# Optimization experiments

Hardware: AMD Instinct MI355X
Metric: run time of the kernel (lower is better)

Reference implementation:

```python
import jax, jax.numpy as jnp
import numpy as np

N_NODES = 50000
N_EDGES = 800000
N_RELS = 200
D = 128


def setup_inputs() -> dict:
    key = jax.random.key(0)
    ks = jax.random.split(key, 9)
    h = jax.random.normal(ks[0], (N_NODES, D), dtype=jnp.float32)
    r = jax.random.normal(ks[1], (N_RELS, D), dtype=jnp.float32)
    norm = jax.random.uniform(ks[2], (N_NODES, 1), dtype=jnp.float32)
    src = jax.random.randint(ks[3], (N_EDGES,), 0, N_NODES, dtype=jnp.int32)
    dst = jax.random.randint(ks[4], (N_EDGES,), 0, N_NODES, dtype=jnp.int32)
    rel = jax.random.randint(ks[5], (N_EDGES,), 0, N_RELS, dtype=jnp.int32)
    stdv = 1.0 / np.sqrt(D)
    W_msg = jax.random.uniform(ks[6], (D, D), minval=-stdv, maxval=stdv, dtype=jnp.float32)
    W = jax.random.uniform(ks[7], (D, D), minval=-stdv, maxval=stdv, dtype=jnp.float32)
    b = jax.random.uniform(ks[8], (D,), minval=-stdv, maxval=stdv, dtype=jnp.float32)
    return {"h": h, "r": r, "norm": norm, "src": src, "dst": dst, "rel": rel,
            "W_msg": W_msg, "W": W, "b": b}


def reference(h, r, norm, src, dst, rel, W_msg, W, b):
    # dropout=0.0 (eval); h = h * norm (symmetric-norm pre-scale)
    hn = h * norm                                    # [N, D]
    # per-edge message: (h_src - r_rel) @ W_msg
    msg = (hn[src] - r[rel]) @ W_msg                 # [E, D]
    # scatter-sum to destination nodes, then post-scale by norm
    agg = jax.ops.segment_sum(msg, dst, num_segments=hn.shape[0]) * norm  # [N, D]
    out = hn @ W + agg + b
    return jax.nn.relu(out)
```

## Files before the change

### kernel.cpp

```cpp
#include <hip/hip_runtime.h>

#define N_NODES 50000
#define N_EDGES 800000
#define DIM 128
#define K2 256
#define NREL 200
#define NB2 391
#define SLAB 3072
#define EPB 2048
#define FILL_BLOCKS ((N_EDGES + EPB - 1) / EPB)
#define BNF 16
#define NFB 3125
#define ECAP6 768

typedef unsigned short u16;
typedef __attribute__((ext_vector_type(8))) short short8;
typedef __attribute__((ext_vector_type(4))) float f32x4;

__device__ __forceinline__ float bf2f(u16 v) {
    union { unsigned int u; float f; } x;
    x.u = ((unsigned int)v) << 16;
    return x.f;
}

__device__ __forceinline__ u16 f2bf(float f) {
    union { unsigned int u; float f; } x;
    x.f = f;
    return (u16)((x.u + 0x7FFFu + ((x.u >> 16) & 1u)) >> 16);
}

__device__ __forceinline__ int sniff_fp32(const void* h, int tid) {
    const u16* hp = (const u16*)h;
    u16 v = hp[2 * (tid & 63)];
    float a = fabsf(bf2f(v));
    int insane = ((v & 0x7F80) == 0x7F80) || (a != 0.0f && (a > 1e6f || a < 1e-20f));
    return __popcll(__ballot(insane)) > 16;
}

#define PREP_H (N_NODES * 32)
#define PREP_R (NREL * 32)
#define PREP_W 8192
#define PREP_N (N_NODES / 4)
#define PREP_B 32
#define PREP_TOT (PREP_H + PREP_R + PREP_W + PREP_N + PREP_B)
#define PREP_BLK512 ((PREP_TOT + 511) / 512)
__global__ __launch_bounds__(512) void prep_fill(
    const void* __restrict__ h, const void* __restrict__ r, const void* __restrict__ norm,
    const void* __restrict__ W, const void* __restrict__ Wmsg, const void* __restrict__ bias,
    const int* __restrict__ dst, const int* __restrict__ src, const int* __restrict__ rel,
    u16* __restrict__ hx, u16* __restrict__ r_bf, u16* __restrict__ wt,
    u16* __restrict__ norm_bf, float* __restrict__ b_f,
    int* __restrict__ cursor, int* __restrict__ spk1)
{
    __shared__ int hist[NB2];
    __shared__ int lbase[NB2];
    __shared__ int gbase[NB2];
    __shared__ int sd[512];
    __shared__ int pay[EPB];
    __shared__ u16 bkt[EPB];
    int tid = threadIdx.x;

    if (blockIdx.x < FILL_BLOCKS) {
        for (int i = tid; i < NB2; i += 512) hist[i] = 0;
        __syncthreads();
        int e0 = blockIdx.x * EPB;
        int myb[4], myr[4], myp[4];
#pragma unroll
        for (int i = 0; i < 4; ++i) {
            int e = e0 + i * 512 + tid;
            myb[i] = -1;
            if (e < N_EDGES) {
                int d = dst[e];
                int b = d >> 7;
                myb[i] = b;
                myr[i] = atomicAdd(&hist[b], 1);
                myp[i] = src[e] | (rel[e] << 16) | ((d & 127) << 24);
            }
        }
        __syncthreads();
        sd[tid] = (tid < NB2) ? hist[tid] : 0;
        __syncthreads();
        for (int off = 1; off < 512; off <<= 1) {
            int v = (tid >= off) ? sd[tid - off] : 0;
            __syncthreads();
            sd[tid] += v;
            __syncthreads();
        }
        if (tid < NB2) {
            lbase[tid] = sd[tid] - hist[tid];
            gbase[tid] = tid * SLAB + (hist[tid] ? atomicAdd(&cursor[tid], hist[tid]) : 0);
        }
        __syncthreads();
#pragma unroll
        for (int i = 0; i < 4; ++i) {
            if (myb[i] >= 0) {
                int lp = lbase[myb[i]] + myr[i];
                pay[lp] = myp[i];
                bkt[lp] = (u16)myb[i];
            }
        }
        __syncthreads();
        int total = N_EDGES - e0; if (total > EPB) total = EPB;
#pragma unroll
        for (int i = 0; i < 4; ++i) {
            int lp = i * 512 + tid;
            if (lp < total) {
                int b = bkt[lp];
                spk1[gbase[b] + (lp - lbase[b])] = pay[lp];
            }
        }
        return;
    }

    int isf = sniff_fp32(h, tid);
    int t = (blockIdx.x - FILL_BLOCKS) * 512 + tid;
    if (t < PREP_H) {
        int n = t >> 5, c = t & 31;
        float4 v; float nv;
        if (isf) {
            nv = ((const float*)norm)[n];
            v = *(const float4*)((const float*)h + (size_t)n * DIM + c * 4);
        } else {
            nv = bf2f(((const u16*)norm)[n]);
            ushort4 u = *(const ushort4*)((const u16*)h + (size_t)n * DIM + c * 4);
            v = make_float4(bf2f(u.x), bf2f(u.y), bf2f(u.z), bf2f(u.w));
        }
        ushort4 o;
        o.x = f2bf(v.x * nv); o.y = f2bf(v.y * nv); o.z = f2bf(v.z * nv); o.w = f2bf(v.w * nv);
        *(ushort4*)(hx + (size_t)n * DIM + c * 4) = o;
    } else if (t < PREP_H + PREP_R) {
        int t2 = t - PREP_H;
        int rho = t2 >> 5, c = t2 & 31;
        float4 v;
        if (isf) v = *(const float4*)((const float*)r + (size_t)rho * DIM + c * 4);
        else {
            ushort4 u = *(const ushort4*)((const u16*)r + (size_t)rho * DIM + c * 4);
            v = make_float4(bf2f(u.x), bf2f(u.y), bf2f(u.z), bf2f(u.w));
        }
        ushort4 o;
        o.x = f2bf(v.x); o.y = f2bf(v.y); o.z = f2bf(v.z); o.w = f2bf(v.w);
        *(ushort4*)(r_bf + (size_t)rho * DIM + c * 4) = o;
    } else if (t < PREP_H + PREP_R + PREP_W) {
        int t3 = t - PREP_H - PREP_R;
        int j = t3 >> 6;
        int k0 = (t3 & 63) * 4;
        ushort4 o;
        u16* op = (u16*)&o;
        for (int kk = 0; kk < 4; ++kk) {
            int k = k0 + kk;
            float wv;
            if (isf) wv = (k < 128) ? ((const float*)W)[(size_t)k * DIM + j]
                                    : ((const float*)Wmsg)[(size_t)(k - 128) * DIM + j];
            else     wv = (k < 128) ? bf2f(((const u16*)W)[(size_t)k * DIM + j])
                                    : bf2f(((const u16*)Wmsg)[(size_t)(k - 128) * DIM + j]);
            op[kk] = f2bf(wv);
        }
        *(ushort4*)(wt + (size_t)j * K2 + k0) = o;
    } else if (t < PREP_H + PREP_R + PREP_W + PREP_N) {
        int n0 = (t - PREP_H - PREP_R - PREP_W) * 4;
        ushort4 o;
        if (isf) {
            float4 v = *(const float4*)((const float*)norm + n0);
            o.x = f2bf(v.x); o.y = f2bf(v.y); o.z = f2bf(v.z); o.w = f2bf(v.w);
        } else {
            o = *(const ushort4*)((const u16*)norm + n0);
        }
        *(ushort4*)(norm_bf + n0) = o;
    } else if (t < PREP_TOT) {
        int j0 = (t - PREP_H - PREP_R - PREP_W - PREP_N) * 4;
        float4 v;
        if (isf) v = *(const float4*)((const float*)bias + j0);
        else {
            ushort4 u = *(const ushort4*)((const u16*)bias + j0);
            v = make_float4(bf2f(u.x), bf2f(u.y), bf2f(u.z), bf2f(u.w));
        }
        *(float4*)(b_f + j0) = v;
    }
}

__global__ __launch_bounds__(512) void sort_fine(
    const int* __restrict__ cursor, const int* __restrict__ spk1,
    int* __restrict__ spk2, int* __restrict__ nodeBase)
{
    __shared__ int hist[128];
    __shared__ int lb[128];
    __shared__ int sd[512];
    __shared__ int sorted[SLAB];
    int tid = threadIdx.x;
    int fb = blockIdx.x;
    int acc = 0;
    for (int i = tid; i < NB2; i += 512)
        if (i < fb) acc += cursor[i];
    sd[tid] = acc;
    __syncthreads();
    for (int off = 256; off > 0; off >>= 1) {
        if (tid < off) sd[tid] += sd[tid + off];
        __syncthreads();
    }
    int base = sd[0];
    int size = cursor[fb];
    if (size > SLAB) size = SLAB;
    if (tid < 128) hist[tid] = 0;
    __syncthreads();
    int myp[6], myr[6], myd[6];
#pragma unroll
    for (int q = 0; q < 6; ++q) {
        int i = tid + q * 512;
        myd[q] = -1;
        if (i < size) {
            int pk = spk1[fb * SLAB + i];
            int dl = (pk >> 24) & 127;
            myp[q] = pk;
            myd[q] = dl;
            myr[q] = atomicAdd(&hist[dl], 1);
        }
    }
    __syncthreads();
    if (tid < 128) sd[tid] = hist[tid];
    __syncthreads();
    for (int off = 1; off < 128; off <<= 1) {
        int v = 0;
        if (tid < 128 && tid >= off) v = sd[tid - off];
        __syncthreads();
        if (tid < 128) sd[tid] += v;
        __syncthreads();
    }
    if (tid < 128) lb[tid] = sd[tid] - hist[tid];
    __syncthreads();
#pragma unroll
    for (int q = 0; q < 6; ++q)
        if (myd[q] >= 0) sorted[lb[myd[q]] + myr[q]] = myp[q];
    __syncthreads();
    for (int i = tid; i < size; i += 512) spk2[base + i] = sorted[i];
    if (tid < 128) {
        int node = fb * 128 + tid;
        if (node <= N_NODES) nodeBase[node] = base + lb[tid];
    }
    if (fb == 0 && tid == 0) nodeBase[N_NODES] = N_EDGES;
}

__global__ __launch_bounds__(256) void bucket_fused(
    const u16* __restrict__ hx, const u16* __restrict__ r_bf,
    const u16* __restrict__ norm_bf, const float* __restrict__ b_f,
    const int* __restrict__ nodeBase, const int* __restrict__ spk,
    const u16* __restrict__ wt, const void* __restrict__ h, void* __restrict__ out)
{
    __shared__ int nb[BNF + 1];
    __shared__ int eidx[ECAP6];
    __shared__ u16 Xu[BNF][136];
    int tid = threadIdx.x;
    int b = blockIdx.x;
    if (tid <= BNF) nb[tid] = nodeBase[b * BNF + tid];
    __syncthreads();
    int bs = nb[0];
    int tot = nb[BNF] - bs; if (tot > ECAP6) tot = ECAP6;
    for (int i = tid; i < tot; i += 256) eidx[i] = spk[bs + i];
    __syncthreads();

    int g = tid & 15, grp = tid >> 4;
    {
        int rs = nb[grp] - bs, re = nb[grp + 1] - bs;
        if (rs > ECAP6) rs = ECAP6;
        if (re > ECAP6) re = ECAP6;
        int cnt = re - rs;
        float acc[8] = {};
        int j = 0;
        for (; j + 3 < cnt; j += 4) {
            int pk0 = eidx[rs + j], pk1 = eidx[rs + j + 1];
            int pk2 = eidx[rs + j + 2], pk3 = eidx[rs + j + 3];
            short8 h0 = *(const short8*)(hx + (size_t)(pk0 & 0xFFFF) * DIM + g * 8);
            short8 h1 = *(const short8*)(hx + (size_t)(pk1 & 0xFFFF) * DIM + g * 8);
            short8 h2 = *(const short8*)(hx + (size_t)(pk2 & 0xFFFF) * DIM + g * 8);
            short8 h3 = *(const short8*)(hx + (size_t)(pk3 & 0xFFFF) * DIM + g * 8);
            short8 v0 = *(const short8*)(r_bf + (size_t)((pk0 >> 16) & 0xFF) * DIM + g * 8);
            short8 v1 = *(const short8*)(r_bf + (size_t)((pk1 >> 16) & 0xFF) * DIM + g * 8);
            short8 v2 = *(const short8*)(r_bf + (size_t)((pk2 >> 16) & 0xFF) * DIM + g * 8);
            short8 v3 = *(const short8*)(r_bf + (size_t)((pk3 >> 16) & 0xFF) * DIM + g * 8);
#pragma unroll
            for (int d = 0; d < 8; ++d) {
                acc[d] += (bf2f((u16)h0[d]) - bf2f((u16)v0[d]))
                        + (bf2f((u16)h1[d]) - bf2f((u16)v1[d]))
                        + (bf2f((u16)h2[d]) - bf2f((u16)v2[d]))
                        + (bf2f((u16)h3[d]) - bf2f((u16)v3[d]));
            }
        }
        for (; j < cnt; ++j) {
            int pk = eidx[rs + j];
            short8 hv = *(const short8*)(hx + (size_t)(pk & 0xFFFF) * DIM + g * 8);
            short8 rv = *(const short8*)(r_bf + (size_t)((pk >> 16) & 0xFF) * DIM + g * 8);
#pragma unroll
            for (int d = 0; d < 8; ++d) acc[d] += bf2f((u16)hv[d]) - bf2f((u16)rv[d]);
        }
        int node = b * BNF + grp;
        float nv = bf2f(norm_bf[node]);
        short8 o;
#pragma unroll
        for (int d = 0; d < 8; ++d) o[d] = (short)f2bf(acc[d] * nv);
        *(short8*)&Xu[grp][g * 8] = o;
    }
    __syncthreads();

    int w = tid >> 6, lane = tid & 63;
    int m = lane & 15, quad = lane >> 4;
    int nodeA = b * BNF + m;
    short8 a[8];
#pragma unroll
    for (int kb = 0; kb < 4; ++kb)
        a[kb] = *(const short8*)(hx + (size_t)nodeA * DIM + kb * 32 + quad * 8);
#pragma unroll
    for (int kb = 0; kb < 4; ++kb)
        a[4 + kb] = *(const short8*)&Xu[m][kb * 32 + quad * 8];
    int isf = sniff_fp32(h, tid);
#pragma unroll
    for (int ct = 0; ct < 2; ++ct) {
        int n0 = w * 32 + ct * 16;
        f32x4 c4 = {0.f, 0.f, 0.f, 0.f};
#pragma unroll
        for (int kb = 0; kb < 8; ++kb) {
            short8 bv = *(const short8*)(wt + (size_t)(n0 + m) * K2 + kb * 32 + quad * 8);
            c4 = __builtin_amdgcn_mfma_f32_16x16x32_bf16(a[kb], bv, c4, 0, 0, 0);
        }
        int col = n0 + m;
        float bb = b_f[col];
#pragma unroll
        for (int rg = 0; rg < 4; ++rg) {
            int n = b * BNF + quad * 4 + rg;
            float v = c4[rg] + bb;
            v = v > 0.f ? v : 0.f;
            if (isf) ((float*)out)[(size_t)n * DIM + col] = v;
            else     ((u16*)out)[(size_t)n * DIM + col] = f2bf(v);
        }
    }
}

static inline size_t alup(size_t x) { return (x + 255) & ~(size_t)255; }

extern "C" void kernel_launch(void* const* d_in, const int* in_sizes, int n_in,
                              void* d_out, int out_size, void* d_ws, size_t ws_size,
                              hipStream_t stream) {
    const void* h    = d_in[0];
    const void* r    = d_in[1];
    const void* norm = d_in[2];
    const int* src   = (const int*)d_in[3];
    const int* dst   = (const int*)d_in[4];
    const int* rel   = (const int*)d_in[5];
    const void* Wmsg = d_in[6];
    const void* W    = d_in[7];
    const void* b    = d_in[8];

    char* p = (char*)d_ws;
    u16* hx       = (u16*)p;                 p += alup((size_t)N_NODES * DIM * 2);
    u16* r_bf     = (u16*)p;                 p += alup((size_t)NREL * DIM * 2);
    u16* wt       = (u16*)p;                 p += alup((size_t)DIM * K2 * 2);
    u16* norm_bf  = (u16*)p;                 p += alup((size_t)N_NODES * 2);
    float* b_f    = (float*)p;               p += alup((size_t)DIM * 4);
    int* cursor   = (int*)p;                 p += alup((size_t)NB2 * 4);
    int* nodeBase = (int*)p;                 p += alup((size_t)(N_NODES + 64) * 4);
    int* spk1     = (int*)p;                 p += alup((size_t)NB2 * SLAB * 4);
    int* spk2     = (int*)p;                 p += alup((size_t)N_EDGES * 4);

    hipMemsetAsync(cursor, 0, (size_t)NB2 * 4, stream);
    prep_fill<<<FILL_BLOCKS + PREP_BLK512, 512, 0, stream>>>(
        h, r, norm, W, Wmsg, b, dst, src, rel,
        hx, r_bf, wt, norm_bf, b_f, cursor, spk1);
    sort_fine<<<NB2, 512, 0, stream>>>(cursor, spk1, spk2, nodeBase);
    bucket_fused<<<NFB, 256, 0, stream>>>(
        hx, r_bf, norm_bf, b_f, nodeBase, spk2, wt, h, d_out);
}
```

Measured before the change: 173.3 us.

## Fuse fine sort into aggregation kernel via per-block shared-memory bucketing

Removes the separate sort_fine kernel and the spk2/nodeBase buffers. Each aggregation block of 16 nodes now scans its coarse 128-node slab and uses shared-memory atomics to bucket the edges for its own 16 nodes, capping each node at DEGCAP=64 edges. This saves one kernel launch and a global write and read of the sorted edge list. In exchange every slab is read 8 times, once per sub-block, and nodes with more than 64 in-edges would be truncated. The order of edges within a node also becomes nondeterministic.

```diff
diff --git a/kernel.cpp b/kernel.cpp
--- a/kernel.cpp
+++ b/kernel.cpp
@@ -9,9 +9,8 @@
 #define SLAB 3072
 #define EPB 2048
 #define FILL_BLOCKS ((N_EDGES + EPB - 1) / EPB)
-#define BNF 16
-#define NFB 3125
-#define ECAP6 768
+#define NFB8 (NB2 * 8)
+#define DEGCAP 64
 
 typedef unsigned short u16;
 typedef __attribute__((ext_vector_type(8))) short short8;
@@ -178,96 +177,43 @@
     }
 }
 
-__global__ __launch_bounds__(512) void sort_fine(
-    const int* __restrict__ cursor, const int* __restrict__ spk1,
-    int* __restrict__ spk2, int* __restrict__ nodeBase)
-{
-    __shared__ int hist[128];
-    __shared__ int lb[128];
-    __shared__ int sd[512];
-    __shared__ int sorted[SLAB];
-    int tid = threadIdx.x;
-    int fb = blockIdx.x;
-    int acc = 0;
-    for (int i = tid; i < NB2; i += 512)
-        if (i < fb) acc += cursor[i];
-    sd[tid] = acc;
-    __syncthreads();
-    for (int off = 256; off > 0; off >>= 1) {
-        if (tid < off) sd[tid] += sd[tid + off];
-        __syncthreads();
-    }
-    int base = sd[0];
-    int size = cursor[fb];
-    if (size > SLAB) size = SLAB;
-    if (tid < 128) hist[tid] = 0;
-    __syncthreads();
-    int myp[6], myr[6], myd[6];
-#pragma unroll
-    for (int q = 0; q < 6; ++q) {
-        int i = tid + q * 512;
-        myd[q] = -1;
-        if (i < size) {
-            int pk = spk1[fb * SLAB + i];
-            int dl = (pk >> 24) & 127;
-            myp[q] = pk;
-            myd[q] = dl;
-            myr[q] = atomicAdd(&hist[dl], 1);
-        }
-    }
-    __syncthreads();
-    if (tid < 128) sd[tid] = hist[tid];
-    __syncthreads();
-    for (int off = 1; off < 128; off <<= 1) {
-        int v = 0;
-        if (tid < 128 && tid >= off) v = sd[tid - off];
-        __syncthreads();
-        if (tid < 128) sd[tid] += v;
-        __syncthreads();
-    }
-    if (tid < 128) lb[tid] = sd[tid] - hist[tid];
-    __syncthreads();
-#pragma unroll
-    for (int q = 0; q < 6; ++q)
-        if (myd[q] >= 0) sorted[lb[myd[q]] + myr[q]] = myp[q];
-    __syncthreads();
-    for (int i = tid; i < size; i += 512) spk2[base + i] = sorted[i];
-    if (tid < 128) {
-        int node = fb * 128 + tid;
-        if (node <= N_NODES) nodeBase[node] = base + lb[tid];
-    }
-    if (fb == 0 && tid == 0) nodeBase[N_NODES] = N_EDGES;
-}
-
 __global__ __launch_bounds__(256) void bucket_fused(
     const u16* __restrict__ hx, const u16* __restrict__ r_bf,
     const u16* __restrict__ norm_bf, const float* __restrict__ b_f,
-    const int* __restrict__ nodeBase, const int* __restrict__ spk,
+    const int* __restrict__ cursor, const int* __restrict__ spk1,
     const u16* __restrict__ wt, const void* __restrict__ h, void* __restrict__ out)
 {
-    __shared__ int nb[BNF + 1];
-    __shared__ int eidx[ECAP6];
-    __shared__ u16 Xu[BNF][136];
+    __shared__ int sorted16[16][DEGCAP];
+    __shared__ int hist16[16];
+    __shared__ u16 Xu[16][136];
     int tid = threadIdx.x;
     int b = blockIdx.x;
-    if (tid <= BNF) nb[tid] = nodeBase[b * BNF + tid];
+    int fb = b >> 3, oct = b & 7;
+    int nodeRow = fb * 128 + oct * 16;
+
+    if (tid < 16) hist16[tid] = 0;
     __syncthreads();
-    int bs = nb[0];
-    int tot = nb[BNF] - bs; if (tot > ECAP6) tot = ECAP6;
-    for (int i = tid; i < tot; i += 256) eidx[i] = spk[bs + i];
+    int cnt = cursor[fb]; if (cnt > SLAB) cnt = SLAB;
+    const int* slab = spk1 + (size_t)fb * SLAB;
+    for (int i = tid; i < cnt; i += 256) {
+        int pk = slab[i];
+        int dl = (pk >> 24) & 127;
+        if ((dl >> 4) == oct) {
+            int rk = atomicAdd(&hist16[dl & 15], 1);
+            if (rk < DEGCAP) sorted16[dl & 15][rk] = pk;
+        }
+    }
     __syncthreads();
 
     int g = tid & 15, grp = tid >> 4;
     {
-        int rs = nb[grp] - bs, re = nb[grp + 1] - bs;
-        if (rs > ECAP6) rs = ECAP6;
-        if (re > ECAP6) re = ECAP6;
-        int cnt = re - rs;
+        int deg = hist16[grp]; if (deg > DEGCAP) deg = DEGCAP;
+        const int* ep = &sorted16[grp][0];
         float acc[8] = {};
         int j = 0;
-        for (; j + 3 < cnt; j += 4) {
-            int pk0 = eidx[rs + j], pk1 = eidx[rs + j + 1];
-            int pk2 = eidx[rs + j + 2], pk3 = eidx[rs + j + 3];
+        for (; j + 3 < deg; j += 4) {
+            int pk0 = ep[j], pk1 = ep[j + 1];
+            int pk2 = ep[j + 2], pk3 = ep[j + 3];
             short8 h0 = *(const short8*)(hx + (size_t)(pk0 & 0xFFFF) * DIM + g * 8);
             short8 h1 = *(const short8*)(hx + (size_t)(pk1 & 0xFFFF) * DIM + g * 8);
             short8 h2 = *(const short8*)(hx + (size_t)(pk2 & 0xFFFF) * DIM + g * 8);
@@ -284,15 +230,15 @@
                         + (bf2f((u16)h3[d]) - bf2f((u16)v3[d]));
             }
         }
-        for (; j < cnt; ++j) {
-            int pk = eidx[rs + j];
+        for (; j < deg; ++j) {
+            int pk = ep[j];
             short8 hv = *(const short8*)(hx + (size_t)(pk & 0xFFFF) * DIM + g * 8);
             short8 rv = *(const short8*)(r_bf + (size_t)((pk >> 16) & 0xFF) * DIM + g * 8);
 #pragma unroll
             for (int d = 0; d < 8; ++d) acc[d] += bf2f((u16)hv[d]) - bf2f((u16)rv[d]);
         }
-        int node = b * BNF + grp;
-        float nv = bf2f(norm_bf[node]);
+        int node = nodeRow + grp;
+        float nv = bf2f(norm_bf[node < N_NODES ? node : 0]);
         short8 o;
 #pragma unroll
         for (int d = 0; d < 8; ++d) o[d] = (short)f2bf(acc[d] * nv);
@@ -302,7 +248,7 @@
 
     int w = tid >> 6, lane = tid & 63;
     int m = lane & 15, quad = lane >> 4;
-    int nodeA = b * BNF + m;
+    int nodeA = nodeRow + m;
     short8 a[8];
 #pragma unroll
     for (int kb = 0; kb < 4; ++kb)
@@ -324,11 +270,13 @@
         float bb = b_f[col];
 #pragma unroll
         for (int rg = 0; rg < 4; ++rg) {
-            int n = b * BNF + quad * 4 + rg;
-            float v = c4[rg] + bb;
-            v = v > 0.f ? v : 0.f;
-            if (isf) ((float*)out)[(size_t)n * DIM + col] = v;
-            else     ((u16*)out)[(size_t)n * DIM + col] = f2bf(v);
+            int n = nodeRow + quad * 4 + rg;
+            if (n < N_NODES) {
+                float v = c4[rg] + bb;
+                v = v > 0.f ? v : 0.f;
+                if (isf) ((float*)out)[(size_t)n * DIM + col] = v;
+                else     ((u16*)out)[(size_t)n * DIM + col] = f2bf(v);
+            }
         }
     }
 }
@@ -355,15 +303,12 @@
     u16* norm_bf  = (u16*)p;                 p += alup((size_t)N_NODES * 2);
     float* b_f    = (float*)p;               p += alup((size_t)DIM * 4);
     int* cursor   = (int*)p;                 p += alup((size_t)NB2 * 4);
-    int* nodeBase = (int*)p;                 p += alup((size_t)(N_NODES + 64) * 4);
     int* spk1     = (int*)p;                 p += alup((size_t)NB2 * SLAB * 4);
-    int* spk2     = (int*)p;                 p += alup((size_t)N_EDGES * 4);
 
     hipMemsetAsync(cursor, 0, (size_t)NB2 * 4, stream);
     prep_fill<<<FILL_BLOCKS + PREP_BLK512, 512, 0, stream>>>(
         h, r, norm, W, Wmsg, b, dst, src, rel,
         hx, r_bf, wt, norm_bf, b_f, cursor, spk1);
-    sort_fine<<<NB2, 512, 0, stream>>>(cursor, spk1, spk2, nodeBase);
-    bucket_fused<<<NFB, 256, 0, stream>>>(
-        hx, r_bf, norm_bf, b_f, nodeBase, spk2, wt, h, d_out);
-}
+    bucket_fused<<<NFB8, 256, 0, stream>>>(
+        hx, r_bf, norm_bf, b_f, cursor, spk1, wt, h, d_out);
+}
```

Measured after the change: 175.8 us. No clear change (+1.4%).

## Balance per-block edge aggregation by splitting edges evenly across thread groups

Applied to the files above, without the earlier changes.

Instead of assigning each 16-thread group one destination node, which leaves groups idle when degrees vary, the block's sorted edge list is split into equal contiguous chunks per group. Groups flush complete node sums straight to shared memory. Partial sums for nodes that straddle chunk boundaries go to a small shared buffer and are combined in a second pass. This targets load imbalance in the gather phase, at the cost of extra shared memory, branching on node changes, and a combine step. It relies on the local node index being packed into the upper bits of each edge key and assumes each group holds at most two boundary partials.

```diff
diff --git a/kernel.cpp b/kernel.cpp
--- a/kernel.cpp
+++ b/kernel.cpp
@@ -248,26 +248,49 @@
     __shared__ int nb[BNF + 1];
     __shared__ int eidx[ECAP6];
     __shared__ u16 Xu[BNF][136];
+    __shared__ float bpart[BNF][2][132];
+    __shared__ int bnode[BNF][2];
     int tid = threadIdx.x;
     int b = blockIdx.x;
     if (tid <= BNF) nb[tid] = nodeBase[b * BNF + tid];
+    if (tid < 32) bnode[tid >> 1][tid & 1] = -1;
     __syncthreads();
     int bs = nb[0];
     int tot = nb[BNF] - bs; if (tot > ECAP6) tot = ECAP6;
     for (int i = tid; i < tot; i += 256) eidx[i] = spk[bs + i];
     __syncthreads();
 
-    int g = tid & 15, grp = tid >> 4;
+    int g = tid & 15, gg = tid >> 4;
+    int q = (tot + 15) >> 4;
+    int lo = gg * q; if (lo > tot) lo = tot;
+    int hi = lo + q; if (hi > tot) hi = tot;
+
     {
-        int rs = nb[grp] - bs, re = nb[grp + 1] - bs;
-        if (rs > ECAP6) rs = ECAP6;
-        if (re > ECAP6) re = ECAP6;
-        int cnt = re - rs;
         float acc[8] = {};
-        int j = 0;
-        for (; j + 3 < cnt; j += 4) {
-            int pk0 = eidx[rs + j], pk1 = eidx[rs + j + 1];
-            int pk2 = eidx[rs + j + 2], pk3 = eidx[rs + j + 3];
+        int cur = -1, nslot = 0;
+        auto flush = [&](int n) {
+            int rs = nb[n] - bs;     if (rs > ECAP6) rs = ECAP6;
+            int re = nb[n + 1] - bs; if (re > ECAP6) re = ECAP6;
+            if (rs >= lo && re <= hi) {
+                float nv = bf2f(norm_bf[b * BNF + n]);
+                short8 o;
+#pragma unroll
+                for (int d = 0; d < 8; ++d) o[d] = (short)f2bf(acc[d] * nv);
+                *(short8*)&Xu[n][g * 8] = o;
+            } else {
+                int s = nslot++;
+#pragma unroll
+                for (int d = 0; d < 8; ++d) bpart[gg][s][g * 8 + d] = acc[d];
+                if (g == 0) bnode[gg][s] = n;
+            }
+#pragma unroll
+            for (int d = 0; d < 8; ++d) acc[d] = 0.f;
+        };
+
+        int j = lo;
+        for (; j + 3 < hi; j += 4) {
+            int pk0 = eidx[j], pk1 = eidx[j + 1];
+            int pk2 = eidx[j + 2], pk3 = eidx[j + 3];
             short8 h0 = *(const short8*)(hx + (size_t)(pk0 & 0xFFFF) * DIM + g * 8);
             short8 h1 = *(const short8*)(hx + (size_t)(pk1 & 0xFFFF) * DIM + g * 8);
             short8 h2 = *(const short8*)(hx + (size_t)(pk2 & 0xFFFF) * DIM + g * 8);
@@ -276,27 +299,61 @@
             short8 v1 = *(const short8*)(r_bf + (size_t)((pk1 >> 16) & 0xFF) * DIM + g * 8);
             short8 v2 = *(const short8*)(r_bf + (size_t)((pk2 >> 16) & 0xFF) * DIM + g * 8);
             short8 v3 = *(const short8*)(r_bf + (size_t)((pk3 >> 16) & 0xFF) * DIM + g * 8);
-#pragma unroll
-            for (int d = 0; d < 8; ++d) {
-                acc[d] += (bf2f((u16)h0[d]) - bf2f((u16)v0[d]))
-                        + (bf2f((u16)h1[d]) - bf2f((u16)v1[d]))
-                        + (bf2f((u16)h2[d]) - bf2f((u16)v2[d]))
-                        + (bf2f((u16)h3[d]) - bf2f((u16)v3[d]));
-            }
-        }
-        for (; j < cnt; ++j) {
-            int pk = eidx[rs + j];
+            int n0 = (pk0 >> 24) & 15, n1 = (pk1 >> 24) & 15;
+            int n2 = (pk2 >> 24) & 15, n3 = (pk3 >> 24) & 15;
+            if (n0 != cur) { if (cur >= 0) flush(cur); cur = n0; }
+#pragma unroll
+            for (int d = 0; d < 8; ++d) acc[d] += bf2f((u16)h0[d]) - bf2f((u16)v0[d]);
+            if (n1 != cur) { flush(cur); cur = n1; }
+#pragma unroll
+            for (int d = 0; d < 8; ++d) acc[d] += bf2f((u16)h1[d]) - bf2f((u16)v1[d]);
+            if (n2 != cur) { flush(cur); cur = n2; }
+#pragma unroll
+            for (int d = 0; d < 8; ++d) acc[d] += bf2f((u16)h2[d]) - bf2f((u16)v2[d]);
+            if (n3 != cur) { flush(cur); cur = n3; }
+#pragma unroll
+            for (int d = 0; d < 8; ++d) acc[d] += bf2f((u16)h3[d]) - bf2f((u16)v3[d]);
+        }
+        for (; j < hi; ++j) {
+            int pk = eidx[j];
             short8 hv = *(const short8*)(hx + (size_t)(pk & 0xFFFF) * DIM + g * 8);
             short8 rv = *(const short8*)(r_bf + (size_t)((pk >> 16) & 0xFF) * DIM + g * 8);
+            int nn = (pk >> 24) & 15;
+            if (nn != cur) { if (cur >= 0) flush(cur); cur = nn; }
 #pragma unroll
             for (int d = 0; d < 8; ++d) acc[d] += bf2f((u16)hv[d]) - bf2f((u16)rv[d]);
         }
-        int node = b * BNF + grp;
-        float nv = bf2f(norm_bf[node]);
-        short8 o;
-#pragma unroll
-        for (int d = 0; d < 8; ++d) o[d] = (short)f2bf(acc[d] * nv);
-        *(short8*)&Xu[grp][g * 8] = o;
+        if (cur >= 0) flush(cur);
+    }
+    __syncthreads();
+
+    {
+        int n = gg;
+        int rs = nb[n] - bs;     if (rs > ECAP6) rs = ECAP6;
+        int re = nb[n + 1] - bs; if (re > ECAP6) re = ECAP6;
+        int empty = (re <= rs);
+        int need = empty;
+        if (!empty) {
+            int gA = rs / q, gB = (re - 1) / q;
+            need = (gA != gB);
+        }
+        if (need) {
+            float a2[8] = {};
+            for (int g2 = 0; g2 < BNF; ++g2) {
+#pragma unroll
+                for (int s = 0; s < 2; ++s) {
+                    if (bnode[g2][s] == n) {
+#pragma unroll
+                        for (int d = 0; d < 8; ++d) a2[d] += bpart[g2][s][g * 8 + d];
+                    }
+                }
+            }
+            float nv = bf2f(norm_bf[b * BNF + n]);
+            short8 o;
+#pragma unroll
+            for (int d = 0; d < 8; ++d) o[d] = (short)f2bf(a2[d] * nv);
+            *(short8*)&Xu[n][g * 8] = o;
+        }
     }
     __syncthreads();
 
```

New measurement: 174.0 us. Within noise of the previous version (+0.4%).

## Replace global-cursor bucket fill with per-block fixed-capacity slots and count matrix

Applied to the files above, without the earlier changes.

The coarse bucketing pass no longer does a block-local prefix scan, staged scatter and global atomic cursor per bucket. Each fill block now writes edges straight into a fixed-capacity slot (CCAP per block per bucket) and records the per-block counts in a byte matrix. The fine sort gathers valid entries through a shared queue, and buckets are laid out at fixed SLAB offsets with a per-bucket end array, so the global prefix sum and the memset disappear. In exchange it relies on capacity caps (26 per block-bucket, 3072 per bucket) that silently drop edges if exceeded, and the fine sort scans a larger, sparse row.

```diff
diff --git a/kernel.cpp b/kernel.cpp
--- a/kernel.cpp
+++ b/kernel.cpp
@@ -7,6 +7,8 @@
 #define NREL 200
 #define NB2 391
 #define SLAB 3072
+#define CCAP 26
+#define ROWW (NB2 * CCAP)
 #define EPB 2048
 #define FILL_BLOCKS ((N_EDGES + EPB - 1) / EPB)
 #define BNF 16
@@ -14,6 +16,7 @@
 #define ECAP6 768
 
 typedef unsigned short u16;
+typedef unsigned char u8;
 typedef __attribute__((ext_vector_type(8))) short short8;
 typedef __attribute__((ext_vector_type(4))) float f32x4;
 
@@ -50,64 +53,32 @@
     const int* __restrict__ dst, const int* __restrict__ src, const int* __restrict__ rel,
     u16* __restrict__ hx, u16* __restrict__ r_bf, u16* __restrict__ wt,
     u16* __restrict__ norm_bf, float* __restrict__ b_f,
-    int* __restrict__ cursor, int* __restrict__ spk1)
+    int* __restrict__ spk1, u8* __restrict__ counts)
 {
     __shared__ int hist[NB2];
-    __shared__ int lbase[NB2];
-    __shared__ int gbase[NB2];
-    __shared__ int sd[512];
-    __shared__ int pay[EPB];
-    __shared__ u16 bkt[EPB];
     int tid = threadIdx.x;
 
     if (blockIdx.x < FILL_BLOCKS) {
+        int blk = blockIdx.x;
         for (int i = tid; i < NB2; i += 512) hist[i] = 0;
         __syncthreads();
-        int e0 = blockIdx.x * EPB;
-        int myb[4], myr[4], myp[4];
+        int e0 = blk * EPB;
 #pragma unroll
         for (int i = 0; i < 4; ++i) {
             int e = e0 + i * 512 + tid;
-            myb[i] = -1;
             if (e < N_EDGES) {
                 int d = dst[e];
                 int b = d >> 7;
-                myb[i] = b;
-                myr[i] = atomicAdd(&hist[b], 1);
-                myp[i] = src[e] | (rel[e] << 16) | ((d & 127) << 24);
+                int rk = atomicAdd(&hist[b], 1);
+                if (rk < CCAP)
+                    spk1[(size_t)b * ROWW + blk * CCAP + rk] =
+                        src[e] | (rel[e] << 16) | ((d & 127) << 24);
             }
         }
         __syncthreads();
-        sd[tid] = (tid < NB2) ? hist[tid] : 0;
-        __syncthreads();
-        for (int off = 1; off < 512; off <<= 1) {
-            int v = (tid >= off) ? sd[tid - off] : 0;
-            __syncthreads();
-            sd[tid] += v;
-            __syncthreads();
-        }
-        if (tid < NB2) {
-            lbase[tid] = sd[tid] - hist[tid];
-            gbase[tid] = tid * SLAB + (hist[tid] ? atomicAdd(&cursor[tid], hist[tid]) : 0);
-        }
-        __syncthreads();
-#pragma unroll
-        for (int i = 0; i < 4; ++i) {
-            if (myb[i] >= 0) {
-                int lp = lbase[myb[i]] + myr[i];
-                pay[lp] = myp[i];
-                bkt[lp] = (u16)myb[i];
-            }
-        }
-        __syncthreads();
-        int total = N_EDGES - e0; if (total > EPB) total = EPB;
-#pragma unroll
-        for (int i = 0; i < 4; ++i) {
-            int lp = i * 512 + tid;
-            if (lp < total) {
-                int b = bkt[lp];
-                spk1[gbase[b] + (lp - lbase[b])] = pay[lp];
-            }
+        for (int i = tid; i < NB2; i += 512) {
+            int c = hist[i]; if (c > CCAP) c = CCAP;
+            counts[(size_t)i * NB2 + blk] = (u8)c;
         }
         return;
     }
@@ -179,43 +150,38 @@
 }
 
 __global__ __launch_bounds__(512) void sort_fine(
-    const int* __restrict__ cursor, const int* __restrict__ spk1,
-    int* __restrict__ spk2, int* __restrict__ nodeBase)
+    const u8* __restrict__ counts, const int* __restrict__ spk1,
+    int* __restrict__ spk2, int* __restrict__ nodeBase, int* __restrict__ bucketEnd)
 {
+    __shared__ int cnt[NB2];
+    __shared__ int queue[SLAB];
+    __shared__ int sorted[SLAB];
     __shared__ int hist[128];
     __shared__ int lb[128];
-    __shared__ int sd[512];
-    __shared__ int sorted[SLAB];
+    __shared__ int cur[128];
+    __shared__ int sd[128];
+    __shared__ int qn;
     int tid = threadIdx.x;
     int fb = blockIdx.x;
-    int acc = 0;
-    for (int i = tid; i < NB2; i += 512)
-        if (i < fb) acc += cursor[i];
-    sd[tid] = acc;
-    __syncthreads();
-    for (int off = 256; off > 0; off >>= 1) {
-        if (tid < off) sd[tid] += sd[tid + off];
-        __syncthreads();
-    }
-    int base = sd[0];
-    int size = cursor[fb];
-    if (size > SLAB) size = SLAB;
+    for (int i = tid; i < NB2; i += 512) cnt[i] = counts[(size_t)fb * NB2 + i];
     if (tid < 128) hist[tid] = 0;
-    __syncthreads();
-    int myp[6], myr[6], myd[6];
-#pragma unroll
-    for (int q = 0; q < 6; ++q) {
-        int i = tid + q * 512;
-        myd[q] = -1;
-        if (i < size) {
-            int pk = spk1[fb * SLAB + i];
-            int dl = (pk >> 24) & 127;
-            myp[q] = pk;
-            myd[q] = dl;
-            myr[q] = atomicAdd(&hist[dl], 1);
-        }
-    }
-    __syncthreads();
+    if (tid == 0) qn = 0;
+    __syncthreads();
+    const int* row = spk1 + (size_t)fb * ROWW;
+    for (int p = tid; p < ROWW; p += 512) {
+        int i = p / CCAP;
+        int k = p - i * CCAP;
+        if (k < cnt[i]) {
+            int pk = row[p];
+            int q = atomicAdd(&qn, 1);
+            if (q < SLAB) {
+                queue[q] = pk;
+                atomicAdd(&hist[(pk >> 24) & 127], 1);
+            }
+        }
+    }
+    __syncthreads();
+    int size = qn; if (size > SLAB) size = SLAB;
     if (tid < 128) sd[tid] = hist[tid];
     __syncthreads();
     for (int off = 1; off < 128; off <<= 1) {
@@ -225,24 +191,30 @@
         if (tid < 128) sd[tid] += v;
         __syncthreads();
     }
-    if (tid < 128) lb[tid] = sd[tid] - hist[tid];
-    __syncthreads();
-#pragma unroll
-    for (int q = 0; q < 6; ++q)
-        if (myd[q] >= 0) sorted[lb[myd[q]] + myr[q]] = myp[q];
-    __syncthreads();
+    if (tid < 128) { lb[tid] = sd[tid] - hist[tid]; cur[tid] = 0; }
+    __syncthreads();
+    for (int i = tid; i < size; i += 512) {
+        int pk = queue[i];
+        int dl = (pk >> 24) & 127;
+        int rk = atomicAdd(&cur[dl], 1);
+        int pos = lb[dl] + rk;
+        if (pos < SLAB) sorted[pos] = pk;
+    }
+    __syncthreads();
+    int base = fb * SLAB;
     for (int i = tid; i < size; i += 512) spk2[base + i] = sorted[i];
     if (tid < 128) {
         int node = fb * 128 + tid;
         if (node <= N_NODES) nodeBase[node] = base + lb[tid];
     }
-    if (fb == 0 && tid == 0) nodeBase[N_NODES] = N_EDGES;
+    if (tid == 0) bucketEnd[fb] = base + size;
 }
 
 __global__ __launch_bounds__(256) void bucket_fused(
     const u16* __restrict__ hx, const u16* __restrict__ r_bf,
     const u16* __restrict__ norm_bf, const float* __restrict__ b_f,
-    const int* __restrict__ nodeBase, const int* __restrict__ spk,
+    const int* __restrict__ nodeBase, const int* __restrict__ bucketEnd,
+    const int* __restrict__ spk,
     const u16* __restrict__ wt, const void* __restrict__ h, void* __restrict__ out)
 {
     __shared__ int nb[BNF + 1];
@@ -250,7 +222,11 @@
     __shared__ u16 Xu[BNF][136];
     int tid = threadIdx.x;
     int b = blockIdx.x;
-    if (tid <= BNF) nb[tid] = nodeBase[b * BNF + tid];
+    if (tid <= BNF) {
+        int v = nodeBase[b * BNF + tid];
+        if (tid == BNF && (b & 7) == 7) v = bucketEnd[b >> 3];
+        nb[tid] = v;
+    }
     __syncthreads();
     int bs = nb[0];
     int tot = nb[BNF] - bs; if (tot > ECAP6) tot = ECAP6;
@@ -354,16 +330,16 @@
     u16* wt       = (u16*)p;                 p += alup((size_t)DIM * K2 * 2);
     u16* norm_bf  = (u16*)p;                 p += alup((size_t)N_NODES * 2);
     float* b_f    = (float*)p;               p += alup((size_t)DIM * 4);
-    int* cursor   = (int*)p;                 p += alup((size_t)NB2 * 4);
     int* nodeBase = (int*)p;                 p += alup((size_t)(N_NODES + 64) * 4);
-    int* spk1     = (int*)p;                 p += alup((size_t)NB2 * SLAB * 4);
-    int* spk2     = (int*)p;                 p += alup((size_t)N_EDGES * 4);
-
-    hipMemsetAsync(cursor, 0, (size_t)NB2 * 4, stream);
+    int* bucketEnd = (int*)p;                p += alup((size_t)NB2 * 4);
+    u8* counts    = (u8*)p;                  p += alup((size_t)NB2 * NB2);
+    int* spk1     = (int*)p;                 p += alup((size_t)NB2 * ROWW * 4);
+    int* spk2     = (int*)p;                 p += alup((size_t)NB2 * SLAB * 4);
+
     prep_fill<<<FILL_BLOCKS + PREP_BLK512, 512, 0, stream>>>(
         h, r, norm, W, Wmsg, b, dst, src, rel,
-        hx, r_bf, wt, norm_bf, b_f, cursor, spk1);
-    sort_fine<<<NB2, 512, 0, stream>>>(cursor, spk1, spk2, nodeBase);
+        hx, r_bf, wt, norm_bf, b_f, spk1, counts);
+    sort_fine<<<NB2, 512, 0, stream>>>(counts, spk1, spk2, nodeBase, bucketEnd);
     bucket_fused<<<NFB, 256, 0, stream>>>(
-        hx, r_bf, norm_bf, b_f, nodeBase, spk2, wt, h, d_out);
-}
+        hx, r_bf, norm_bf, b_f, nodeBase, bucketEnd, spk2, wt, h, d_out);
+}
```

After: 173.2 us. No clear change (-0.1%).
